# Optimization experiments

Measured on AMD Instinct MI355X. Metric: run time of the kernel, lower is better.

The kernel has to match this reference:

```python
import jax, jax.numpy as jnp
import numpy as np

LN_EPS = 1e-5
NORM_EPS = 1e-12


def entmax15_last(x):
    """Exact 1.5-entmax over the last axis (Peters & Martins sort algorithm)."""
    d = x.shape[-1]
    x = x / 2.0
    x = x - jnp.max(x, axis=-1, keepdims=True)
    xs = jnp.sort(x, axis=-1)[..., ::-1]  # descending
    k = jnp.arange(1, d + 1, dtype=x.dtype)
    mean = jnp.cumsum(xs, axis=-1) / k
    meansq = jnp.cumsum(xs * xs, axis=-1) / k
    ss = k * (meansq - jnp.square(mean))
    delta = (1.0 - ss) / k
    tau = mean - jnp.sqrt(jnp.clip(delta, 0.0))
    support = (tau <= xs).astype(jnp.int32)
    k_star = jnp.sum(support, axis=-1, keepdims=True) - 1  # last valid index
    tau_star = jnp.take_along_axis(tau, k_star, axis=-1)
    return jnp.square(jnp.maximum(x - tau_star, 0.0))


def layer_norm(x, gamma, beta):
    mu = jnp.mean(x, axis=-1, keepdims=True)
    var = jnp.mean(jnp.square(x - mu), axis=-1, keepdims=True)
    return (x - mu) / jnp.sqrt(var + LN_EPS) * gamma + beta


def setup_inputs() -> dict:
    key = jax.random.key(0)
    ks = jax.random.split(key, 4)
    B, M, N, D, T, L = 256, 64, 32, 128, 64, 128
    return {
        "x": jax.random.normal(ks[0], (B, M, D), dtype=jnp.float32),
        "route_weights": jax.random.normal(ks[1], (M, N, D, T), dtype=jnp.float32),
        "thread": jax.random.uniform(ks[2], (1, M, N), dtype=jnp.float32),
        "routing_leaves": jax.random.uniform(ks[3], (L, T), dtype=jnp.float32),
        "ln_gamma": jnp.ones((T,), dtype=jnp.float32),
        "ln_beta": jnp.zeros((T,), dtype=jnp.float32),
    }


def reference(x, route_weights, thread, routing_leaves, ln_gamma, ln_beta):
    # entmax15 over dim=-2 (the in_capsule_size axis D) of route_weights [M,N,D,T]
    w = jnp.swapaxes(route_weights, -1, -2)
    w = entmax15_last(w)
    weights = jnp.swapaxes(w, -1, -2)
    # priors: [B, M, N, T]
    priors = jnp.einsum('bmd,mndt->bmnt', x, weights)
    # routing
    leave_hash = routing_leaves / jnp.maximum(
        jnp.linalg.norm(routing_leaves, axis=-1, keepdims=True), NORM_EPS)
    votes = jax.nn.sigmoid(jnp.einsum('ld,bmnt->bmnl', leave_hash, priors)) if False else \
        jax.nn.sigmoid(jnp.einsum('ld,bmnd->bmnl', leave_hash, priors))  # [B,M,N,L]
    mean_cap = jnp.mean(votes, axis=1, keepdims=True)
    dis = jnp.mean(jnp.square(votes - mean_cap), axis=-1)  # [B,M,N]
    weight = jax.nn.relu(jnp.square(thread) - dis)
    prob = jax.nn.softmax(weight, axis=-2)  # over M (in capsules)
    next_caps = jnp.sum(prob[:, :, :, None] * priors, axis=1)  # [B,N,T]
    return layer_norm(next_caps, ln_gamma, ln_beta)
```

## Files before the change

### kernel.cpp

```cpp
#include <hip/hip_runtime.h>
#include <hip/hip_bf16.h>
#include <math.h>

#define B_ 256
#define M_ 64
#define N_ 32
#define D_ 128
#define T_ 64
#define L_ 128

typedef __attribute__((ext_vector_type(8))) short short8;
typedef __attribute__((ext_vector_type(4))) float floatx4;

__device__ __forceinline__ unsigned short f2bf(float f) {
  unsigned int u = __float_as_uint(f);
  unsigned int r = (u + 0x7fffu + ((u >> 16) & 1u)) >> 16;
  return (unsigned short)r;
}
__device__ __forceinline__ float bf2f(unsigned short s) {
  return __uint_as_float(((unsigned int)s) << 16);
}
__device__ __forceinline__ float frcp(float x) { return __builtin_amdgcn_rcpf(x); }
__device__ __forceinline__ unsigned pk2bf(float a, float b) {
  __hip_bfloat162 h = __float22bfloat162_rn(make_float2(a, b));
  unsigned u;
  __builtin_memcpy(&u, &h, 4);
  return u;
}

__global__ __launch_bounds__(256) void k_prep(const float* __restrict__ x,
                                              const float* __restrict__ leaves,
                                              unsigned short* __restrict__ xb2,
                                              unsigned short* __restrict__ lhn,
                                              const float* __restrict__ thr,
                                              float* __restrict__ thrT) {
  const int tid = threadIdx.x;
  const int bx = blockIdx.x;
  if (bx < 1024) {
    int idx = bx * 256 + tid;
    int j = idx & 15, b = (idx >> 4) & 255, m = idx >> 12;
    const float* xs = x + ((size_t)b * M_ + m) * D_ + j;
    float v[8];
#pragma unroll
    for (int i = 0; i < 8; ++i) v[i] = xs[i * 16];
    unsigned short* dst = xb2 + ((size_t)m * B_ + b) * D_ + j * 8;
    uint4 w;
    w.x = pk2bf(v[0], v[1]);
    w.y = pk2bf(v[2], v[3]);
    w.z = pk2bf(v[4], v[5]);
    w.w = pk2bf(v[6], v[7]);
    *(uint4*)dst = w;
  } else if (bx == 1024) {
    if (tid < L_) {
      const float* r = leaves + tid * T_;
      float ss = 0.f;
      for (int i = 0; i < T_; ++i) ss = fmaf(r[i], r[i], ss);
      float inv = frcp(fmaxf(sqrtf(ss), 1e-12f));
      unsigned short* o = lhn + tid * T_;
      for (int i = 0; i < T_; ++i) o[i] = f2bf(r[i] * inv);
    }
  } else {
#pragma unroll
    for (int k = 0; k < 8; ++k) {
      int idx = k * 256 + tid;
      int nn = idx >> 6, mm = idx & 63;
      thrT[idx] = thr[mm * N_ + nn];
    }
  }
}

#define BS_STRIDE 136
__global__ __launch_bounds__(256, 4) void k_wpriors(const unsigned short* __restrict__ xb2,
                                                    const float* __restrict__ rw,
                                                    unsigned short* __restrict__ priors) {
  const int m = blockIdx.x, n = blockIdx.y;
  const int tid = threadIdx.x;
  const int wid = tid >> 6, lane = tid & 63;
  const int row16 = lane & 15, quad = lane >> 4;

  __shared__ __align__(16) unsigned short Bs[64 * BS_STRIDE];
  __shared__ __align__(16) unsigned short Ct[128 * 72];

  short8 xfr[2][2][4];
#pragma unroll
  for (int sub = 0; sub < 2; ++sub) {
    const int b = wid * 32 + sub * 16 + row16;
    const unsigned short* xptr = xb2 + ((size_t)m * B_ + b) * D_ + quad * 8;
#pragma unroll
    for (int ks = 0; ks < 4; ++ks) xfr[0][sub][ks] = *(const short8*)(xptr + ks * 32);
  }

  {
    const int g = tid >> 4, j = tid & 15;
    const float* base = rw + (size_t)(m * N_ + n) * (D_ * T_) + g * 4;
    floatx4 xv[8];
#pragma unroll
    for (int i = 0; i < 8; ++i)
      xv[i] = *(const floatx4*)(base + (size_t)(i * 16 + j) * T_);

    floatx4 mx = xv[0];
#pragma unroll
    for (int i = 1; i < 8; ++i)
#pragma unroll
      for (int c = 0; c < 4; ++c) mx[c] = fmaxf(mx[c], xv[i][c]);
#pragma unroll
    for (int off = 1; off <= 8; off <<= 1)
#pragma unroll
      for (int c = 0; c < 4; ++c) mx[c] = fmaxf(mx[c], __shfl_xor(mx[c], off));
#pragma unroll
    for (int i = 0; i < 8; ++i)
#pragma unroll
      for (int c = 0; c < 4; ++c) xv[i][c] = (xv[i][c] - mx[c]) * 0.5f;

    floatx4 lo = (floatx4){-1.f, -1.f, -1.f, -1.f};
    floatx4 hi = (floatx4){0.f, 0.f, 0.f, 0.f};
    for (int it = 0; it < 8; ++it) {
      floatx4 tau, f = (floatx4){0.f, 0.f, 0.f, 0.f};
#pragma unroll
      for (int c = 0; c < 4; ++c) tau[c] = 0.5f * (lo[c] + hi[c]);
#pragma unroll
      for (int i = 0; i < 8; ++i)
#pragma unroll
        for (int c = 0; c < 4; ++c) {
          float u = fmaxf(xv[i][c] - tau[c], 0.0f);
          f[c] = fmaf(u, u, f[c]);
        }
#pragma unroll
      for (int off = 1; off <= 8; off <<= 1)
#pragma unroll
        for (int c = 0; c < 4; ++c) f[c] += __shfl_xor(f[c], off);
#pragma unroll
      for (int c = 0; c < 4; ++c) {
        bool ge = f[c] >= 1.0f;
        lo[c] = ge ? tau[c] : lo[c];
        hi[c] = ge ? hi[c] : tau[c];
      }
    }
    floatx4 tau0, cnt = (floatx4){0,0,0,0}, s1 = (floatx4){0,0,0,0}, s2 = (floatx4){0,0,0,0};
#pragma unroll
    for (int c = 0; c < 4; ++c) tau0[c] = 0.5f * (lo[c] + hi[c]);
#pragma unroll
    for (int i = 0; i < 8; ++i)
#pragma unroll
      for (int c = 0; c < 4; ++c) {
        bool in = xv[i][c] > tau0[c];
        float q = in ? xv[i][c] : 0.0f;
        cnt[c] += in ? 1.0f : 0.0f;
        s1[c] += q;
        s2[c] = fmaf(q, q, s2[c]);
      }
#pragma unroll
    for (int off = 1; off <= 8; off <<= 1)
#pragma unroll
      for (int c = 0; c < 4; ++c) {
        cnt[c] += __shfl_xor(cnt[c], off);
        s1[c] += __shfl_xor(s1[c], off);
        s2[c] += __shfl_xor(s2[c], off);
      }
    floatx4 tau;
#pragma unroll
    for (int c = 0; c < 4; ++c) {
      float rc = frcp(cnt[c]);
      float mean = s1[c] * rc;
      float ss = s2[c] - mean * s1[c];
      float delta = (1.0f - ss) * rc;
      tau[c] = mean - sqrtf(fmaxf(delta, 0.0f));
    }

#pragma unroll
    for (int c = 0; c < 4; ++c) {
      float u[8];
#pragma unroll
      for (int i = 0; i < 8; ++i) {
        float v = fmaxf(xv[i][c] - tau[c], 0.0f);
        u[i] = v * v;
      }
      uint4 w;
      w.x = pk2bf(u[0], u[1]);
      w.y = pk2bf(u[2], u[3]);
      w.z = pk2bf(u[4], u[5]);
      w.w = pk2bf(u[6], u[7]);
      *(uint4*)&Bs[(g * 4 + c) * BS_STRIDE + j * 8] = w;
    }
  }

#pragma unroll
  for (int sub = 0; sub < 2; ++sub) {
    const int b = 128 + wid * 32 + sub * 16 + row16;
    const unsigned short* xptr = xb2 + ((size_t)m * B_ + b) * D_ + quad * 8;
#pragma unroll
    for (int ks = 0; ks < 4; ++ks) xfr[1][sub][ks] = *(const short8*)(xptr + ks * 32);
  }
  __syncthreads();

#pragma unroll
  for (int c = 0; c < 2; ++c) {
    floatx4 acc[2][4];
#pragma unroll
    for (int sub = 0; sub < 2; ++sub)
#pragma unroll
      for (int cf = 0; cf < 4; ++cf) acc[sub][cf] = (floatx4){0.f, 0.f, 0.f, 0.f};

#pragma unroll
    for (int cf = 0; cf < 4; ++cf) {
      short8 afr[4];
#pragma unroll
      for (int ks = 0; ks < 4; ++ks)
        afr[ks] = *(const short8*)&Bs[(cf * 16 + row16) * BS_STRIDE + ks * 32 + quad * 8];
#pragma unroll
      for (int ks = 0; ks < 4; ++ks)
#pragma unroll
        for (int sub = 0; sub < 2; ++sub)
          acc[sub][cf] = __builtin_amdgcn_mfma_f32_16x16x32_bf16(afr[ks], xfr[c][sub][ks], acc[sub][cf], 0, 0, 0);
    }

    if (c) __syncthreads();
#pragma unroll
    for (int sub = 0; sub < 2; ++sub)
#pragma unroll
      for (int cf = 0; cf < 4; ++cf) {
        uint2 o2;
        o2.x = pk2bf(acc[sub][cf][0], acc[sub][cf][1]);
        o2.y = pk2bf(acc[sub][cf][2], acc[sub][cf][3]);
        *(uint2*)&Ct[(wid * 32 + sub * 16 + row16) * 72 + cf * 16 + quad * 4] = o2;
      }
    __syncthreads();

    {
      int q = tid >> 4, s = tid & 15;
      int row = q * 8 + (s >> 1);
      int half = s & 1;
      int b = c * 128 + row;
      const unsigned short* src = &Ct[row * 72 + half * 32];
      unsigned short* dst = priors + (((size_t)n * B_ + b) * M_ + m) * T_ + half * 32;
      uint4 a0 = *(const uint4*)(src);
      uint4 a1 = *(const uint4*)(src + 8);
      uint4 a2 = *(const uint4*)(src + 16);
      uint4 a3 = *(const uint4*)(src + 24);
      *(uint4*)(dst) = a0;
      *(uint4*)(dst + 8) = a1;
      *(uint4*)(dst + 16) = a2;
      *(uint4*)(dst + 24) = a3;
    }
  }
}

__global__ __launch_bounds__(256, 4) void k_route(const unsigned short* __restrict__ priors,
                                                  const unsigned short* __restrict__ lhn,
                                                  const float* __restrict__ thrT,
                                                  const float* __restrict__ gamma,
                                                  const float* __restrict__ beta,
                                                  float* __restrict__ out) {
  const int n = blockIdx.x, g4 = blockIdx.y;
  const int tid = threadIdx.x;
  const int wid = tid >> 6, lane = tid & 63;
  const int col = lane & 15, quad = lane >> 4;

  __shared__ float probL[4][64];

  const int b = g4 * 4 + wid;

  const unsigned short* base = priors + ((size_t)n * B_ + b) * (M_ * T_);
  short8 afr[4][2];
#pragma unroll
  for (int mt = 0; mt < 4; ++mt)
#pragma unroll
    for (int ks = 0; ks < 2; ++ks)
      afr[mt][ks] = *(const short8*)(base + (mt * 16 + col) * T_ + ks * 32 + quad * 8);

  float thv = thrT[n * 64 + lane];

  float dis[4][4];
#pragma unroll
  for (int mt = 0; mt < 4; ++mt)
#pragma unroll
    for (int r = 0; r < 4; ++r) dis[mt][r] = 0.f;

#pragma unroll
  for (int s4 = 0; s4 < 4; ++s4) {
    floatx4 acc[4][2];
#pragma unroll
    for (int mt = 0; mt < 4; ++mt)
#pragma unroll
      for (int lt = 0; lt < 2; ++lt) acc[mt][lt] = (floatx4){0.f, 0.f, 0.f, 0.f};

#pragma unroll
    for (int lt = 0; lt < 2; ++lt) {
#pragma unroll
      for (int ks = 0; ks < 2; ++ks) {
        short8 bfr = *(const short8*)(lhn + (s4 * 32 + lt * 16 + col) * T_ + ks * 32 + quad * 8);
#pragma unroll
        for (int mt = 0; mt < 4; ++mt)
          acc[mt][lt] = __builtin_amdgcn_mfma_f32_16x16x32_bf16(afr[mt][ks], bfr, acc[mt][lt], 0, 0, 0);
      }
    }

#pragma unroll
    for (int mt = 0; mt < 4; ++mt)
#pragma unroll
      for (int lt = 0; lt < 2; ++lt)
#pragma unroll
        for (int r = 0; r < 4; ++r)
          acc[mt][lt][r] = frcp(1.0f + __expf(-acc[mt][lt][r]));

    float mc[2];
#pragma unroll
    for (int lt = 0; lt < 2; ++lt) {
      float s = 0.f;
#pragma unroll
      for (int mt = 0; mt < 4; ++mt)
#pragma unroll
        for (int r = 0; r < 4; ++r) s += acc[mt][lt][r];
      s += __shfl_xor(s, 16);
      s += __shfl_xor(s, 32);
      mc[lt] = s * (1.0f / 64.0f);
    }

#pragma unroll
    for (int mt = 0; mt < 4; ++mt)
#pragma unroll
      for (int r = 0; r < 4; ++r) {
        float s = 0.f;
#pragma unroll
        for (int lt = 0; lt < 2; ++lt) {
          float df = acc[mt][lt][r] - mc[lt];
          s = fmaf(df, df, s);
        }
        dis[mt][r] += s;
      }
  }

#pragma unroll
  for (int off = 1; off <= 8; off <<= 1)
#pragma unroll
    for (int mt = 0; mt < 4; ++mt)
#pragma unroll
      for (int r = 0; r < 4; ++r) dis[mt][r] += __shfl_xor(dis[mt][r], off);

  float e[4][4];
  float mxw = 0.f;
#pragma unroll
  for (int mt = 0; mt < 4; ++mt)
#pragma unroll
    for (int r = 0; r < 4; ++r) {
      float th = __shfl(thv, mt * 16 + quad * 4 + r);
      float w = fmaxf(th * th - dis[mt][r] * (1.0f / 128.0f), 0.0f);
      e[mt][r] = w;
      mxw = fmaxf(mxw, w);
    }
  mxw = fmaxf(mxw, __shfl_xor(mxw, 16));
  mxw = fmaxf(mxw, __shfl_xor(mxw, 32));
  float ssum = 0.f;
#pragma unroll
  for (int mt = 0; mt < 4; ++mt)
#pragma unroll
    for (int r = 0; r < 4; ++r) {
      e[mt][r] = __expf(e[mt][r] - mxw);
      ssum += e[mt][r];
    }
  ssum += __shfl_xor(ssum, 16);
  ssum += __shfl_xor(ssum, 32);
  float inv = frcp(ssum);
  if (col == 0) {
#pragma unroll
    for (int mt = 0; mt < 4; ++mt)
#pragma unroll
      for (int r = 0; r < 4; ++r)
        probL[wid][mt * 16 + quad * 4 + r] = e[mt][r] * inv;
  }

  float pr[4];
#pragma unroll
  for (int mt = 0; mt < 4; ++mt) pr[mt] = probL[wid][mt * 16 + col];

  float o[2][8];
#pragma unroll
  for (int ks = 0; ks < 2; ++ks)
#pragma unroll
    for (int j = 0; j < 8; ++j) o[ks][j] = 0.f;
#pragma unroll
  for (int mt = 0; mt < 4; ++mt)
#pragma unroll
    for (int ks = 0; ks < 2; ++ks)
#pragma unroll
      for (int j = 0; j < 8; ++j)
        o[ks][j] = fmaf(pr[mt], bf2f((unsigned short)afr[mt][ks][j]), o[ks][j]);
#pragma unroll
  for (int off = 1; off <= 8; off <<= 1)
#pragma unroll
    for (int ks = 0; ks < 2; ++ks)
#pragma unroll
      for (int j = 0; j < 8; ++j) o[ks][j] += __shfl_xor(o[ks][j], off);

  float mu = 0.f;
#pragma unroll
  for (int ks = 0; ks < 2; ++ks)
#pragma unroll
    for (int j = 0; j < 8; ++j) mu += o[ks][j];
  mu += __shfl_xor(mu, 16);
  mu += __shfl_xor(mu, 32);
  mu *= (1.0f / 64.0f);
  float var = 0.f;
#pragma unroll
  for (int ks = 0; ks < 2; ++ks)
#pragma unroll
    for (int j = 0; j < 8; ++j) {
      float d = o[ks][j] - mu;
      o[ks][j] = d;
      var = fmaf(d, d, var);
    }
  var += __shfl_xor(var, 16);
  var += __shfl_xor(var, 32);
  var *= (1.0f / 64.0f);
  float rstd = rsqrtf(var + 1e-5f);

  if (col == 0) {
    float* obase = out + ((size_t)b * N_ + n) * T_;
#pragma unroll
    for (int ks = 0; ks < 2; ++ks) {
      int tb = ks * 32 + quad * 8;
      float4 g0 = *(const float4*)(gamma + tb);
      float4 g1 = *(const float4*)(gamma + tb + 4);
      float4 b0 = *(const float4*)(beta + tb);
      float4 b1 = *(const float4*)(beta + tb + 4);
      float4 r0, r1;
      r0.x = o[ks][0] * rstd * g0.x + b0.x;
      r0.y = o[ks][1] * rstd * g0.y + b0.y;
      r0.z = o[ks][2] * rstd * g0.z + b0.z;
      r0.w = o[ks][3] * rstd * g0.w + b0.w;
      r1.x = o[ks][4] * rstd * g1.x + b1.x;
      r1.y = o[ks][5] * rstd * g1.y + b1.y;
      r1.z = o[ks][6] * rstd * g1.z + b1.z;
      r1.w = o[ks][7] * rstd * g1.w + b1.w;
      *(float4*)(obase + tb) = r0;
      *(float4*)(obase + tb + 4) = r1;
    }
  }
}

extern "C" void kernel_launch(void* const* d_in, const int* in_sizes, int n_in,
                              void* d_out, int out_size, void* d_ws, size_t ws_size,
                              hipStream_t stream) {
  const float* x = (const float*)d_in[0];
  const float* rw = (const float*)d_in[1];
  const float* thr = (const float*)d_in[2];
  const float* leaves = (const float*)d_in[3];
  const float* gamma = (const float*)d_in[4];
  const float* beta = (const float*)d_in[5];
  float* out = (float*)d_out;

  char* ws = (char*)d_ws;
  unsigned short* priors = (unsigned short*)(ws);
  unsigned short* xb2 = (unsigned short*)(ws + 67108864);
  unsigned short* lhn = (unsigned short*)(ws + 71303168);
  float* thrT = (float*)(ws + 71319552);

  hipLaunchKernelGGL(k_prep, dim3(1026), dim3(256), 0, stream, x, leaves, xb2, lhn, thr, thrT);
  hipLaunchKernelGGL(k_wpriors, dim3(64, 32), dim3(256), 0, stream, xb2, rw, priors);
  hipLaunchKernelGGL(k_route, dim3(32, 64), dim3(256), 0, stream, priors, lhn, thrT, gamma, beta, out);
}
```

Measured before the change: 177.3 us.

## Replace LDS output staging with cross-lane shuffles and raise occupancy in k_wpriors

```diff
diff --git a/kernel.cpp b/kernel.cpp
--- a/kernel.cpp
+++ b/kernel.cpp
@@ -70,7 +70,7 @@
 }
 
 #define BS_STRIDE 136
-__global__ __launch_bounds__(256, 4) void k_wpriors(const unsigned short* __restrict__ xb2,
+__global__ __launch_bounds__(256, 8) void k_wpriors(const unsigned short* __restrict__ xb2,
                                                     const float* __restrict__ rw,
                                                     unsigned short* __restrict__ priors) {
   const int m = blockIdx.x, n = blockIdx.y;
@@ -79,16 +79,6 @@
   const int row16 = lane & 15, quad = lane >> 4;
 
   __shared__ __align__(16) unsigned short Bs[64 * BS_STRIDE];
-  __shared__ __align__(16) unsigned short Ct[128 * 72];
-
-  short8 xfr[2][2][4];
-#pragma unroll
-  for (int sub = 0; sub < 2; ++sub) {
-    const int b = wid * 32 + sub * 16 + row16;
-    const unsigned short* xptr = xb2 + ((size_t)m * B_ + b) * D_ + quad * 8;
-#pragma unroll
-    for (int ks = 0; ks < 4; ++ks) xfr[0][sub][ks] = *(const short8*)(xptr + ks * 32);
-  }
 
   {
     const int g = tid >> 4, j = tid & 15;
@@ -183,64 +173,60 @@
       *(uint4*)&Bs[(g * 4 + c) * BS_STRIDE + j * 8] = w;
     }
   }
-
-#pragma unroll
-  for (int sub = 0; sub < 2; ++sub) {
-    const int b = 128 + wid * 32 + sub * 16 + row16;
-    const unsigned short* xptr = xb2 + ((size_t)m * B_ + b) * D_ + quad * 8;
-#pragma unroll
-    for (int ks = 0; ks < 4; ++ks) xfr[1][sub][ks] = *(const short8*)(xptr + ks * 32);
-  }
   __syncthreads();
 
 #pragma unroll
   for (int c = 0; c < 2; ++c) {
-    floatx4 acc[2][4];
-#pragma unroll
-    for (int sub = 0; sub < 2; ++sub)
-#pragma unroll
-      for (int cf = 0; cf < 4; ++cf) acc[sub][cf] = (floatx4){0.f, 0.f, 0.f, 0.f};
-
-#pragma unroll
-    for (int cf = 0; cf < 4; ++cf) {
-      short8 afr[4];
-#pragma unroll
-      for (int ks = 0; ks < 4; ++ks)
-        afr[ks] = *(const short8*)&Bs[(cf * 16 + row16) * BS_STRIDE + ks * 32 + quad * 8];
-#pragma unroll
-      for (int ks = 0; ks < 4; ++ks)
-#pragma unroll
-        for (int sub = 0; sub < 2; ++sub)
-          acc[sub][cf] = __builtin_amdgcn_mfma_f32_16x16x32_bf16(afr[ks], xfr[c][sub][ks], acc[sub][cf], 0, 0, 0);
-    }
-
-    if (c) __syncthreads();
-#pragma unroll
-    for (int sub = 0; sub < 2; ++sub)
+#pragma unroll
+    for (int sub = 0; sub < 2; ++sub) {
+      const int b = c * 128 + wid * 32 + sub * 16 + row16;
+      const unsigned short* xptr = xb2 + ((size_t)m * B_ + b) * D_ + quad * 8;
+      short8 xfr[4];
+#pragma unroll
+      for (int ks = 0; ks < 4; ++ks) xfr[ks] = *(const short8*)(xptr + ks * 32);
+
+      floatx4 acc[4];
+#pragma unroll
+      for (int cf = 0; cf < 4; ++cf) acc[cf] = (floatx4){0.f, 0.f, 0.f, 0.f};
 #pragma unroll
       for (int cf = 0; cf < 4; ++cf) {
-        uint2 o2;
-        o2.x = pk2bf(acc[sub][cf][0], acc[sub][cf][1]);
-        o2.y = pk2bf(acc[sub][cf][2], acc[sub][cf][3]);
-        *(uint2*)&Ct[(wid * 32 + sub * 16 + row16) * 72 + cf * 16 + quad * 4] = o2;
-      }
-    __syncthreads();
-
-    {
-      int q = tid >> 4, s = tid & 15;
-      int row = q * 8 + (s >> 1);
-      int half = s & 1;
-      int b = c * 128 + row;
-      const unsigned short* src = &Ct[row * 72 + half * 32];
-      unsigned short* dst = priors + (((size_t)n * B_ + b) * M_ + m) * T_ + half * 32;
-      uint4 a0 = *(const uint4*)(src);
-      uint4 a1 = *(const uint4*)(src + 8);
-      uint4 a2 = *(const uint4*)(src + 16);
-      uint4 a3 = *(const uint4*)(src + 24);
-      *(uint4*)(dst) = a0;
-      *(uint4*)(dst + 8) = a1;
-      *(uint4*)(dst + 16) = a2;
-      *(uint4*)(dst + 24) = a3;
+        short8 afr[4];
+#pragma unroll
+        for (int ks = 0; ks < 4; ++ks)
+          afr[ks] = *(const short8*)&Bs[(cf * 16 + row16) * BS_STRIDE + ks * 32 + quad * 8];
+#pragma unroll
+        for (int ks = 0; ks < 4; ++ks)
+          acc[cf] = __builtin_amdgcn_mfma_f32_16x16x32_bf16(afr[ks], xfr[ks], acc[cf], 0, 0, 0);
+      }
+
+      unsigned X0x = pk2bf(acc[0][0], acc[0][1]), X0y = pk2bf(acc[0][2], acc[0][3]);
+      unsigned X1x = pk2bf(acc[1][0], acc[1][1]), X1y = pk2bf(acc[1][2], acc[1][3]);
+      unsigned X2x = pk2bf(acc[2][0], acc[2][1]), X2y = pk2bf(acc[2][2], acc[2][3]);
+      unsigned X3x = pk2bf(acc[3][0], acc[3][1]), X3y = pk2bf(acc[3][2], acc[3][3]);
+
+      const bool hi2 = (quad & 2) != 0;
+      unsigned s0x = hi2 ? X0x : X2x, s0y = hi2 ? X0y : X2y;
+      unsigned s1x = hi2 ? X1x : X3x, s1y = hi2 ? X1y : X3y;
+      unsigned r0x = __shfl_xor(s0x, 32), r0y = __shfl_xor(s0y, 32);
+      unsigned r1x = __shfl_xor(s1x, 32), r1y = __shfl_xor(s1y, 32);
+      unsigned A0x = hi2 ? r0x : X0x, A0y = hi2 ? r0y : X0y;
+      unsigned A1x = hi2 ? r1x : X1x, A1y = hi2 ? r1y : X1y;
+      unsigned A2x = hi2 ? X2x : r0x, A2y = hi2 ? X2y : r0y;
+      unsigned A3x = hi2 ? X3x : r1x, A3y = hi2 ? X3y : r1y;
+      const bool odd = (quad & 1) != 0;
+      unsigned t0x = odd ? A0x : A1x, t0y = odd ? A0y : A1y;
+      unsigned t1x = odd ? A2x : A3x, t1y = odd ? A2y : A3y;
+      unsigned u0x = __shfl_xor(t0x, 16), u0y = __shfl_xor(t0y, 16);
+      unsigned u1x = __shfl_xor(t1x, 16), u1y = __shfl_xor(t1y, 16);
+      uint4 w0, w1;
+      w0.x = odd ? u0x : A0x;  w0.y = odd ? u0y : A0y;
+      w0.z = odd ? A1x : u0x;  w0.w = odd ? A1y : u0y;
+      w1.x = odd ? u1x : A2x;  w1.y = odd ? u1y : A2y;
+      w1.z = odd ? A3x : u1x;  w1.w = odd ? A3y : u1y;
+
+      unsigned short* dst = priors + (((size_t)n * B_ + b) * M_ + m) * T_ + quad * 16;
+      *(uint4*)dst = w0;
+      *(uint4*)(dst + 8) = w1;
     }
   }
 }
```

Measured after the change: 168.2 us. -5.1%, faster.
